# Optimization experiments

Hardware: AMD Instinct MI355X
Metric: run time of the kernel (lower is better)

Reference implementation:

```python
import jax, jax.numpy as jnp
import numpy as np

NUM_HEADS = 8
DIM_HEAD = 48
SCALE = DIM_HEAD ** -0.5


def setup_inputs() -> dict:
    key = jax.random.key(0)
    k1, k2, k3 = jax.random.split(key, 3)
    B, N, D = 4, 2048, 384
    inner = NUM_HEADS * DIM_HEAD  # 384
    x = jax.random.normal(k1, (B, N, D), dtype=jnp.float32)
    # store weights in [in, out] layout (equivalent to torch Linear W.T)
    Wqkv = jax.random.normal(k2, (D, 3 * inner), dtype=jnp.float32) * (D ** -0.5)
    Wproj = jax.random.normal(k3, (inner, D), dtype=jnp.float32) * (inner ** -0.5)
    bproj = jnp.zeros((D,), dtype=jnp.float32)
    return {"x": x, "Wqkv": Wqkv, "Wproj": Wproj, "bproj": bproj}


def reference(x, Wqkv, Wproj, bproj):
    B, N, D = x.shape
    h, dh = NUM_HEADS, DIM_HEAD
    C = h * dh
    # fused QKV projection (qkv_bias=False)
    qkv = (x @ Wqkv).reshape(B, N, 3, h, dh)
    q = qkv[:, :, 0].transpose(0, 2, 1, 3)  # [B, h, N, dh]
    k = qkv[:, :, 1].transpose(0, 2, 1, 3)
    v = qkv[:, :, 2].transpose(0, 2, 1, 3)
    # naive attention: materialize [B, h, N, N] scores
    sim = jnp.einsum("bhqd,bhkd->bhqk", q, k) * SCALE
    attn = jax.nn.softmax(sim, axis=-1)
    out = jnp.einsum("bhqk,bhkd->bhqd", attn, v)  # [B, h, N, dh]
    out = out.transpose(0, 2, 1, 3).reshape(B, N, C)
    return out @ Wproj + bproj
```

## Files before the change

### kernel.cpp

```cpp
#include <hip/hip_runtime.h>
#include <hip/hip_bf16.h>


typedef _Float16 f16x8 __attribute__((ext_vector_type(8)));
typedef _Float16 f16x4 __attribute__((ext_vector_type(4)));
typedef float    f32x4 __attribute__((ext_vector_type(4)));
typedef float    f32x16 __attribute__((ext_vector_type(16)));

#define QSCL 0.20822035963448658f

__global__ __launch_bounds__(256) void prep(const float* __restrict__ wq,
                                            const float* __restrict__ wp,
                                            _Float16* __restrict__ wqt,
                                            _Float16* __restrict__ wpt)
{
    __shared__ _Float16 t[64][65];
    const int blk = blockIdx.x, tid = threadIdx.x;
    const float* src; _Float16* dst; int Nn, k0, n0;
    if (blk < 108) {
        src = wq; dst = wqt; Nn = 1152;
        k0 = (blk % 6) * 64; n0 = (blk / 6) * 64;
    } else {
        const int b2 = blk - 108;
        src = wp; dst = wpt; Nn = 384;
        k0 = (b2 % 6) * 64; n0 = (b2 / 6) * 64;
    }
    #pragma unroll
    for (int i = 0; i < 16; i++) {
        const int id = tid + i * 256;
        const int k = id >> 6, n = id & 63;
        t[k][n] = (_Float16)src[(size_t)(k0 + k) * Nn + n0 + n];
    }
    __syncthreads();
    #pragma unroll
    for (int i = 0; i < 16; i++) {
        const int id = tid + i * 256;
        const int n = id >> 6, k = id & 63;
        dst[(size_t)(n0 + n) * 384 + k0 + k] = t[k][n];
    }
}

union QkvSmem {
    struct { _Float16 As[128][72]; _Float16 Bs[64][72]; } g;
    _Float16 Ts[64][136];
    _Float16 Ts2[128][72];
};

__global__ __launch_bounds__(256) void qkv_f16(const float* __restrict__ X,
                                               const _Float16* __restrict__ Bt,
                                               _Float16* __restrict__ qh,
                                               _Float16* __restrict__ kh,
                                               _Float16* __restrict__ vt)
{
    __shared__ QkvSmem sm;
    const int tid = threadIdx.x;
    const int w = tid >> 6, lane = tid & 63, cl = lane & 15, quad = lane >> 4;
    const int bm = blockIdx.x, bn = blockIdx.y;

    f32x4 acc[2][4];
    const f32x4 z4 = {0.f, 0.f, 0.f, 0.f};
    #pragma unroll
    for (int mi = 0; mi < 2; mi++)
        #pragma unroll
        for (int t = 0; t < 4; t++) acc[mi][t] = z4;

    const int ar = tid >> 3, ac = (tid & 7) * 8;
    const float*    Ag = X  + (size_t)(bm * 128 + ar) * 384 + ac;
    const _Float16* Bg = Bt + (size_t)(bn * 64  + ar) * 384 + ac;

    float4 pa0[4], pa1[4];
    f16x8 pb[2];
    #pragma unroll
    for (int j = 0; j < 4; j++) {
        pa0[j] = *(const float4*)(Ag + (size_t)(32 * j) * 384);
        pa1[j] = *(const float4*)(Ag + (size_t)(32 * j) * 384 + 4);
    }
    #pragma unroll
    for (int j = 0; j < 2; j++) pb[j] = *(const f16x8*)(Bg + (size_t)(32 * j) * 384);

    for (int k0 = 0; k0 < 384; k0 += 64) {
        __syncthreads();
        #pragma unroll
        for (int j = 0; j < 4; j++) {
            f16x8 hh;
            hh[0] = (_Float16)pa0[j].x; hh[1] = (_Float16)pa0[j].y;
            hh[2] = (_Float16)pa0[j].z; hh[3] = (_Float16)pa0[j].w;
            hh[4] = (_Float16)pa1[j].x; hh[5] = (_Float16)pa1[j].y;
            hh[6] = (_Float16)pa1[j].z; hh[7] = (_Float16)pa1[j].w;
            *(f16x8*)&sm.g.As[ar + 32 * j][ac] = hh;
        }
        #pragma unroll
        for (int j = 0; j < 2; j++) *(f16x8*)&sm.g.Bs[ar + 32 * j][ac] = pb[j];
        __syncthreads();
        if (k0 + 64 < 384) {
            #pragma unroll
            for (int j = 0; j < 4; j++) {
                pa0[j] = *(const float4*)(Ag + (size_t)(32 * j) * 384 + k0 + 64);
                pa1[j] = *(const float4*)(Ag + (size_t)(32 * j) * 384 + k0 + 68);
            }
            #pragma unroll
            for (int j = 0; j < 2; j++)
                pb[j] = *(const f16x8*)(Bg + (size_t)(32 * j) * 384 + k0 + 64);
        }
        #pragma unroll
        for (int kh2 = 0; kh2 < 2; kh2++) {
            f16x8 bf[4];
            #pragma unroll
            for (int t = 0; t < 4; t++)
                bf[t] = *(const f16x8*)&sm.g.Bs[t * 16 + cl][kh2 * 32 + quad * 8];
            #pragma unroll
            for (int mi = 0; mi < 2; mi++) {
                const f16x8 af = *(const f16x8*)&sm.g.As[w * 32 + mi * 16 + cl][kh2 * 32 + quad * 8];
                #pragma unroll
                for (int t = 0; t < 4; t++)
                    acc[mi][t] = __builtin_amdgcn_mfma_f32_16x16x32_f16(af, bf[t], acc[mi][t], 0, 0, 0);
            }
        }
    }

    const int s = (bn * 64) / 384;
    if (s == 2) {
        __syncthreads();
        #pragma unroll
        for (int t = 0; t < 4; t++)
            #pragma unroll
            for (int mi = 0; mi < 2; mi++)
                #pragma unroll
                for (int r = 0; r < 4; r++)
                    sm.Ts[t * 16 + cl][w * 32 + mi * 16 + quad * 4 + r] =
                        (_Float16)acc[mi][t][r];
        __syncthreads();
        const int colbase = bn * 64 - 768;
        const int b  = (bm * 128) >> 11;
        const int n0 = (bm * 128) & 2047;
        #pragma unroll
        for (int i = 0; i < 4; i++) {
            const int c = i * 256 + tid;
            const int col = c >> 4, nc = c & 15;
            const int gcol = colbase + col;
            const int head = gcol / 48, d = gcol - head * 48;
            const int bh = b * 8 + head;
            *(f16x8*)&vt[(size_t)(bh * 48 + d) * 2048 + n0 + nc * 8] =
                *(const f16x8*)&sm.Ts[col][nc * 8];
        }
    } else {
        __syncthreads();
        const float scl = (s == 0) ? QSCL : 1.0f;
        #pragma unroll
        for (int t = 0; t < 4; t++)
            #pragma unroll
            for (int mi = 0; mi < 2; mi++)
                #pragma unroll
                for (int r = 0; r < 4; r++)
                    sm.Ts2[w * 32 + mi * 16 + quad * 4 + r][t * 16 + cl] =
                        (_Float16)(acc[mi][t][r] * scl);
        __syncthreads();
        _Float16* dst = (s == 0) ? qh : kh;
        const int colbase = bn * 64 - s * 384;
        const int b  = (bm * 128) >> 11;
        const int n0 = (bm * 128) & 2047;
        #pragma unroll
        for (int i = 0; i < 4; i++) {
            const int c = i * 256 + tid;
            const int row = c >> 3, ch = c & 7;
            const int gcol = colbase + ch * 8;
            const int head = gcol / 48, d = gcol - head * 48;
            const int bh = b * 8 + head;
            *(f16x8*)&dst[(size_t)(bh * 2048 + n0 + row) * 48 + d] =
                *(const f16x8*)&sm.Ts2[row][ch * 8];
        }
    }
}

__global__ __launch_bounds__(256) void attn_f16(const _Float16* __restrict__ qh,
                                                const _Float16* __restrict__ kh,
                                                const _Float16* __restrict__ vt,
                                                _Float16* __restrict__ ab)
{
    __shared__ _Float16 Ks[64][56];
    __shared__ _Float16 Vts[64][72];
    __shared__ _Float16 Ps[128][72];
    const int tid = threadIdx.x;
    const int w = tid >> 6, lane = tid & 63, ln = lane & 31, h = lane >> 5;
    const int bh = blockIdx.x, qt = blockIdx.y;

    for (int i = tid; i < 16 * 72; i += 256) {
        const int r = 48 + i / 72, c = i - (i / 72) * 72;
        Vts[r][c] = (r == 48) ? (_Float16)1.0f : (_Float16)0.0f;
    }

    f16x8 qf[3];
    {
        const _Float16* qp = qh + (size_t)(bh * 2048 + qt * 128 + w * 32 + ln) * 48 + 8 * h;
        qf[0] = *(const f16x8*)qp;
        qf[1] = *(const f16x8*)(qp + 16);
        qf[2] = *(const f16x8*)(qp + 32);
    }

    f32x16 o0, o1;
    #pragma unroll
    for (int r = 0; r < 16; r++) { o0[r] = 0.f; o1[r] = 0.f; }

    const _Float16* kbase = kh + (size_t)bh * 2048 * 48;
    const _Float16* vbase = vt + (size_t)bh * 48 * 2048;

    const int kr0 = tid / 6,         kc0 = (tid % 6) * 8;
    const int kid1 = tid + 256;
    const int kr1 = kid1 / 6,        kc1 = (kid1 % 6) * 8;
    const int vr0 = tid >> 3,        vc0 = (tid & 7) * 8;
    const int vr1 = (tid + 256) >> 3;
    const _Float16* ks0 = kbase + (size_t)kr0 * 48 + kc0;
    const _Float16* ks1 = kbase + (size_t)kr1 * 48 + kc1;
    const _Float16* vs0 = vbase + (size_t)vr0 * 2048 + vc0;
    const _Float16* vs1 = vbase + (size_t)vr1 * 2048 + vc0;

    f16x8 rk0 = *(const f16x8*)ks0;
    f16x8 rv0 = *(const f16x8*)vs0;
    f16x8 rk1, rv1;
    if (tid < 128) { rk1 = *(const f16x8*)ks1; rv1 = *(const f16x8*)vs1; }

    for (int kt = 0; kt < 2048; kt += 64) {
        __syncthreads();
        *(f16x8*)&Ks[kr0][kc0]  = rk0;
        *(f16x8*)&Vts[vr0][vc0] = rv0;
        if (tid < 128) {
            *(f16x8*)&Ks[kr1][kc1]  = rk1;
            *(f16x8*)&Vts[vr1][vc0] = rv1;
        }
        __syncthreads();
        if (kt + 64 < 2048) {
            rk0 = *(const f16x8*)(ks0 + (size_t)(kt + 64) * 48);
            rv0 = *(const f16x8*)(vs0 + kt + 64);
            if (tid < 128) {
                rk1 = *(const f16x8*)(ks1 + (size_t)(kt + 64) * 48);
                rv1 = *(const f16x8*)(vs1 + kt + 64);
            }
        }

        f32x16 s0, s1;
        #pragma unroll
        for (int r = 0; r < 16; r++) { s0[r] = 0.f; s1[r] = 0.f; }
        #pragma unroll
        for (int i = 0; i < 3; i++) {
            const f16x8 ka0 = *(const f16x8*)&Ks[ln][16 * i + 8 * h];
            s0 = __builtin_amdgcn_mfma_f32_32x32x16_f16(ka0, qf[i], s0, 0, 0, 0);
            const f16x8 ka1 = *(const f16x8*)&Ks[32 + ln][16 * i + 8 * h];
            s1 = __builtin_amdgcn_mfma_f32_32x32x16_f16(ka1, qf[i], s1, 0, 0, 0);
        }

        #pragma unroll
        for (int q = 0; q < 4; q++) {
            f16x4 pk;
            pk[0] = (_Float16)exp2f(s0[4 * q + 0]);
            pk[1] = (_Float16)exp2f(s0[4 * q + 1]);
            pk[2] = (_Float16)exp2f(s0[4 * q + 2]);
            pk[3] = (_Float16)exp2f(s0[4 * q + 3]);
            *(f16x4*)&Ps[w * 32 + ln][8 * q + 4 * h] = pk;
            f16x4 pk1;
            pk1[0] = (_Float16)exp2f(s1[4 * q + 0]);
            pk1[1] = (_Float16)exp2f(s1[4 * q + 1]);
            pk1[2] = (_Float16)exp2f(s1[4 * q + 2]);
            pk1[3] = (_Float16)exp2f(s1[4 * q + 3]);
            *(f16x4*)&Ps[w * 32 + ln][32 + 8 * q + 4 * h] = pk1;
        }

        #pragma unroll
        for (int i = 0; i < 4; i++) {
            const f16x8 pa = *(const f16x8*)&Ps[w * 32 + ln][16 * i + 8 * h];
            const f16x8 v0 = *(const f16x8*)&Vts[ln][16 * i + 8 * h];
            o0 = __builtin_amdgcn_mfma_f32_32x32x16_f16(pa, v0, o0, 0, 0, 0);
            const f16x8 v1 = *(const f16x8*)&Vts[32 + ln][16 * i + 8 * h];
            o1 = __builtin_amdgcn_mfma_f32_32x32x16_f16(pa, v1, o1, 0, 0, 0);
        }
    }

    const int b = bh >> 3, hd = bh & 7;
    #pragma unroll
    for (int r = 0; r < 16; r++) {
        const float lr = __shfl(o1[r], (lane & 32) + 16);
        const float inv = 1.f / lr;
        const int q = qt * 128 + w * 32 + (r & 3) + 8 * (r >> 2) + 4 * h;
        _Float16* orow = ab + (size_t)(b * 2048 + q) * 384 + hd * 48;
        orow[ln] = (_Float16)(o0[r] * inv);
        if (ln < 16) orow[32 + ln] = (_Float16)(o1[r] * inv);
    }
}

__global__ __launch_bounds__(256) void proj_f16(const _Float16* __restrict__ A,
                                                const _Float16* __restrict__ Bt,
                                                const float* __restrict__ bias,
                                                float* __restrict__ out)
{
    __shared__ _Float16 As[64][72];
    __shared__ _Float16 Bs[64][72];
    const int tid = threadIdx.x;
    const int w = tid >> 6, lane = tid & 63, cl = lane & 15, quad = lane >> 4;
    const int bm = blockIdx.x, bn = blockIdx.y;

    f32x4 acc[4];
    const f32x4 z4 = {0.f, 0.f, 0.f, 0.f};
    #pragma unroll
    for (int t = 0; t < 4; t++) acc[t] = z4;

    const int ar = tid >> 3, ac = (tid & 7) * 8;
    const _Float16* Ag = A  + (size_t)(bm * 64 + ar) * 384 + ac;
    const _Float16* Bg = Bt + (size_t)(bn * 64 + ar) * 384 + ac;

    f16x8 pa[2], pb[2];
    #pragma unroll
    for (int j = 0; j < 2; j++) {
        pa[j] = *(const f16x8*)(Ag + (size_t)(32 * j) * 384);
        pb[j] = *(const f16x8*)(Bg + (size_t)(32 * j) * 384);
    }

    for (int k0 = 0; k0 < 384; k0 += 64) {
        __syncthreads();
        #pragma unroll
        for (int j = 0; j < 2; j++) {
            *(f16x8*)&As[ar + 32 * j][ac] = pa[j];
            *(f16x8*)&Bs[ar + 32 * j][ac] = pb[j];
        }
        __syncthreads();
        if (k0 + 64 < 384) {
            #pragma unroll
            for (int j = 0; j < 2; j++) {
                pa[j] = *(const f16x8*)(Ag + (size_t)(32 * j) * 384 + k0 + 64);
                pb[j] = *(const f16x8*)(Bg + (size_t)(32 * j) * 384 + k0 + 64);
            }
        }
        #pragma unroll
        for (int kh2 = 0; kh2 < 2; kh2++) {
            const f16x8 af = *(const f16x8*)&As[w * 16 + cl][kh2 * 32 + quad * 8];
            #pragma unroll
            for (int t = 0; t < 4; t++) {
                const f16x8 bf = *(const f16x8*)&Bs[t * 16 + cl][kh2 * 32 + quad * 8];
                acc[t] = __builtin_amdgcn_mfma_f32_16x16x32_f16(af, bf, acc[t], 0, 0, 0);
            }
        }
    }

    #pragma unroll
    for (int t = 0; t < 4; t++) {
        const int col = bn * 64 + t * 16 + cl;
        const float bv = bias[col];
        #pragma unroll
        for (int r = 0; r < 4; r++) {
            const int row = bm * 64 + w * 16 + quad * 4 + r;
            out[(size_t)row * 384 + col] = acc[t][r] + bv;
        }
    }
}

extern "C" void kernel_launch(void* const* d_in, const int* in_sizes, int n_in,
                              void* d_out, int out_size, void* d_ws, size_t ws_size,
                              hipStream_t stream) {
    const float* x     = (const float*)d_in[0];
    const float* Wqkv  = (const float*)d_in[1];
    const float* Wproj = (const float*)d_in[2];
    const float* bproj = (const float*)d_in[3];
    float* out = (float*)d_out;

    char* ws = (char*)d_ws;
    _Float16* wqkvt  = (_Float16*)(ws + 0);
    _Float16* wprojt = (_Float16*)(ws + 884736);
    _Float16* qh     = (_Float16*)(ws + 1179648);
    _Float16* kh     = (_Float16*)(ws + 7471104);
    _Float16* vt     = (_Float16*)(ws + 13762560);
    _Float16* ab     = (_Float16*)(ws + 20054016);

    prep<<<144, 256, 0, stream>>>(Wqkv, Wproj, wqkvt, wprojt);
    qkv_f16<<<dim3(64, 18), 256, 0, stream>>>(x, wqkvt, qh, kh, vt);
    attn_f16<<<dim3(32, 16), 256, 0, stream>>>(qh, kh, vt, ab);
    proj_f16<<<dim3(128, 6), 256, 0, stream>>>(ab, wprojt, bproj, out);
}
```

Measured before the change: 152.6 us.

## Keep softmax probabilities in registers by transposing PV MFMA and permuting V smem

The attention kernel no longer writes exp'd scores to a shared Ps buffer and reads them back. The PV product is computed transposed (V as the A operand, P from registers as the B operand), and V is stored into shared memory with a permuted column order so the register layout of P matches the MFMA input. The output is then staged through a shared-memory transpose buffer (unioned with K/V) and written with coalesced 16-byte stores instead of scattered scalar stores. This removes the per-tile LDS round trip for P, lowers LDS footprint, and improves output coalescing, at the cost of an index permutation that must exactly match the MFMA lane layout.

```diff
diff --git a/kernel.cpp b/kernel.cpp
--- a/kernel.cpp
+++ b/kernel.cpp
@@ -172,21 +172,27 @@
     }
 }
 
+union AttnSmem {
+    struct {
+        _Float16 Ks[64][56];
+        _Float16 Vts[64][72];
+    } a;
+    _Float16 Ot[128][58];
+};
+
 __global__ __launch_bounds__(256) void attn_f16(const _Float16* __restrict__ qh,
                                                 const _Float16* __restrict__ kh,
                                                 const _Float16* __restrict__ vt,
                                                 _Float16* __restrict__ ab)
 {
-    __shared__ _Float16 Ks[64][56];
-    __shared__ _Float16 Vts[64][72];
-    __shared__ _Float16 Ps[128][72];
+    __shared__ AttnSmem sm;
     const int tid = threadIdx.x;
     const int w = tid >> 6, lane = tid & 63, ln = lane & 31, h = lane >> 5;
     const int bh = blockIdx.x, qt = blockIdx.y;
 
     for (int i = tid; i < 16 * 72; i += 256) {
         const int r = 48 + i / 72, c = i - (i / 72) * 72;
-        Vts[r][c] = (r == 48) ? (_Float16)1.0f : (_Float16)0.0f;
+        sm.a.Vts[r][c] = (r == 48) ? (_Float16)1.0f : (_Float16)0.0f;
     }
 
     f16x8 qf[3];
@@ -209,6 +215,7 @@
     const int kr1 = kid1 / 6,        kc1 = (kid1 % 6) * 8;
     const int vr0 = tid >> 3,        vc0 = (tid & 7) * 8;
     const int vr1 = (tid + 256) >> 3;
+    const int vslot_lo = 16 * ((tid & 7) >> 1) + 4 * (tid & 1);
     const _Float16* ks0 = kbase + (size_t)kr0 * 48 + kc0;
     const _Float16* ks1 = kbase + (size_t)kr1 * 48 + kc1;
     const _Float16* vs0 = vbase + (size_t)vr0 * 2048 + vc0;
@@ -221,11 +228,17 @@
 
     for (int kt = 0; kt < 2048; kt += 64) {
         __syncthreads();
-        *(f16x8*)&Ks[kr0][kc0]  = rk0;
-        *(f16x8*)&Vts[vr0][vc0] = rv0;
+        *(f16x8*)&sm.a.Ks[kr0][kc0] = rk0;
+        {
+            const f16x4* rvh = (const f16x4*)&rv0;
+            *(f16x4*)&sm.a.Vts[vr0][vslot_lo]     = rvh[0];
+            *(f16x4*)&sm.a.Vts[vr0][vslot_lo + 8] = rvh[1];
+        }
         if (tid < 128) {
-            *(f16x8*)&Ks[kr1][kc1]  = rk1;
-            *(f16x8*)&Vts[vr1][vc0] = rv1;
+            *(f16x8*)&sm.a.Ks[kr1][kc1] = rk1;
+            const f16x4* rvh = (const f16x4*)&rv1;
+            *(f16x4*)&sm.a.Vts[vr1][vslot_lo]     = rvh[0];
+            *(f16x4*)&sm.a.Vts[vr1][vslot_lo + 8] = rvh[1];
         }
         __syncthreads();
         if (kt + 64 < 2048) {
@@ -242,47 +255,49 @@
         for (int r = 0; r < 16; r++) { s0[r] = 0.f; s1[r] = 0.f; }
         #pragma unroll
         for (int i = 0; i < 3; i++) {
-            const f16x8 ka0 = *(const f16x8*)&Ks[ln][16 * i + 8 * h];
+            const f16x8 ka0 = *(const f16x8*)&sm.a.Ks[ln][16 * i + 8 * h];
             s0 = __builtin_amdgcn_mfma_f32_32x32x16_f16(ka0, qf[i], s0, 0, 0, 0);
-            const f16x8 ka1 = *(const f16x8*)&Ks[32 + ln][16 * i + 8 * h];
+            const f16x8 ka1 = *(const f16x8*)&sm.a.Ks[32 + ln][16 * i + 8 * h];
             s1 = __builtin_amdgcn_mfma_f32_32x32x16_f16(ka1, qf[i], s1, 0, 0, 0);
         }
 
-        #pragma unroll
-        for (int q = 0; q < 4; q++) {
-            f16x4 pk;
-            pk[0] = (_Float16)exp2f(s0[4 * q + 0]);
-            pk[1] = (_Float16)exp2f(s0[4 * q + 1]);
-            pk[2] = (_Float16)exp2f(s0[4 * q + 2]);
-            pk[3] = (_Float16)exp2f(s0[4 * q + 3]);
-            *(f16x4*)&Ps[w * 32 + ln][8 * q + 4 * h] = pk;
-            f16x4 pk1;
-            pk1[0] = (_Float16)exp2f(s1[4 * q + 0]);
-            pk1[1] = (_Float16)exp2f(s1[4 * q + 1]);
-            pk1[2] = (_Float16)exp2f(s1[4 * q + 2]);
-            pk1[3] = (_Float16)exp2f(s1[4 * q + 3]);
-            *(f16x4*)&Ps[w * 32 + ln][32 + 8 * q + 4 * h] = pk1;
-        }
-
-        #pragma unroll
-        for (int i = 0; i < 4; i++) {
-            const f16x8 pa = *(const f16x8*)&Ps[w * 32 + ln][16 * i + 8 * h];
-            const f16x8 v0 = *(const f16x8*)&Vts[ln][16 * i + 8 * h];
-            o0 = __builtin_amdgcn_mfma_f32_32x32x16_f16(pa, v0, o0, 0, 0, 0);
-            const f16x8 v1 = *(const f16x8*)&Vts[32 + ln][16 * i + 8 * h];
-            o1 = __builtin_amdgcn_mfma_f32_32x32x16_f16(pa, v1, o1, 0, 0, 0);
-        }
-    }
-
+        f16x8 pbf[4];
+        #pragma unroll
+        for (int j = 0; j < 8; j++) {
+            pbf[0][j] = (_Float16)exp2f(s0[j]);
+            pbf[1][j] = (_Float16)exp2f(s0[8 + j]);
+            pbf[2][j] = (_Float16)exp2f(s1[j]);
+            pbf[3][j] = (_Float16)exp2f(s1[8 + j]);
+        }
+
+        #pragma unroll
+        for (int c = 0; c < 4; c++) {
+            const f16x8 av0 = *(const f16x8*)&sm.a.Vts[ln][16 * c + 8 * h];
+            o0 = __builtin_amdgcn_mfma_f32_32x32x16_f16(av0, pbf[c], o0, 0, 0, 0);
+            const f16x8 av1 = *(const f16x8*)&sm.a.Vts[32 + ln][16 * c + 8 * h];
+            o1 = __builtin_amdgcn_mfma_f32_32x32x16_f16(av1, pbf[c], o1, 0, 0, 0);
+        }
+    }
+
+    const float lr  = __shfl(o1[8], ln);
+    const float inv = 1.f / lr;
+
+    __syncthreads();
+    #pragma unroll
+    for (int r = 0; r < 16; r++)
+        sm.Ot[w * 32 + ln][(r & 3) + 8 * (r >> 2) + 4 * h] = (_Float16)(o0[r] * inv);
+    #pragma unroll
+    for (int r = 0; r < 8; r++)
+        sm.Ot[w * 32 + ln][32 + (r & 3) + 8 * (r >> 2) + 4 * h] = (_Float16)(o1[r] * inv);
+    __syncthreads();
     const int b = bh >> 3, hd = bh & 7;
     #pragma unroll
-    for (int r = 0; r < 16; r++) {
-        const float lr = __shfl(o1[r], (lane & 32) + 16);
-        const float inv = 1.f / lr;
-        const int q = qt * 128 + w * 32 + (r & 3) + 8 * (r >> 2) + 4 * h;
-        _Float16* orow = ab + (size_t)(b * 2048 + q) * 384 + hd * 48;
-        orow[ln] = (_Float16)(o0[r] * inv);
-        if (ln < 16) orow[32 + ln] = (_Float16)(o1[r] * inv);
+    for (int i = 0; i < 3; i++) {
+        const int c2 = i * 256 + tid;
+        const int row = c2 / 6, ch = c2 % 6;
+        const int q = qt * 128 + row;
+        *(f16x8*)&ab[(size_t)(b * 2048 + q) * 384 + hd * 48 + ch * 8] =
+            *(const f16x8*)&sm.Ot[row][ch * 8];
     }
 }
 
```

Result: faster. 149.5 us (-2.0%).
